# Kernel tuning notes

Hardware: AMD Instinct MI355X
Metric: run time of the kernel (lower is better)

Reference implementation:

```python
import jax, jax.numpy as jnp
import numpy as np

EPS = 1e-8


def setup_inputs() -> dict:
    key = jax.random.key(0)
    k1, k2, k3 = jax.random.split(key, 3)
    B, K, L, D = 4, 64, 128, 768
    context = jax.random.normal(k1, (B, K, 2, L, D), dtype=jnp.float32)
    # MlpModule(input_size=D): Linear(D, D) -> ReLU -> Linear(D, 1)
    w1 = jax.random.normal(k2, (D, D), dtype=jnp.float32) * (1.0 / np.sqrt(D))
    b1 = jnp.zeros((D,), dtype=jnp.float32)
    w2 = jax.random.normal(k3, (D, 1), dtype=jnp.float32) * (1.0 / np.sqrt(D))
    b2 = jnp.zeros((1,), dtype=jnp.float32)
    return {"context": context, "w1": w1, "b1": b1, "w2": w2, "b2": b2}


def reference(context, w1, b1, w2, b2):
    # context: [B, K, 2, L, D]; slice 0 = context tokens, slice 1 = entity tokens
    ctx = context[:, :, 0, :, :]   # [B, K, L, D]
    ent = context[:, :, 1, :, :]   # [B, K, L, D]

    ctx_norm = jnp.linalg.norm(ctx, axis=-1, keepdims=True)  # [B, K, L, 1]
    ent_norm = jnp.linalg.norm(ent, axis=-1, keepdims=True)  # [B, K, L, 1]

    # cosine-similarity score matrix: [B, K, L, L]
    denom = ctx_norm * jnp.swapaxes(ent_norm, -1, -2) + EPS
    scores = jnp.einsum('bkld,bkmd->bklm', ctx, ent) / denom

    # normalized embeddings (torch code does in-place /= before the stack)
    ctx_n = ctx / ctx_norm
    ent_n = ent / ent_norm

    # top-1 match along entity axis, gather matched entity token per context token
    argmax_idx = jnp.argmax(scores, axis=-1)                       # [B, K, L] int
    matched = jnp.take_along_axis(ent_n, argmax_idx[..., None], axis=2)  # [B, K, L, D]

    pair = jnp.stack([ctx_n, matched], axis=-2)  # [B, K, L, 2, D]

    # MLP: Linear(D,D) -> ReLU -> Linear(D,1), then sum over the pair axis
    h = jax.nn.relu(jnp.einsum('bklpd,de->bklpe', pair, w1) + b1)
    out = jnp.einsum('bklpd,do->bklpo', h, w2) + b2   # [B, K, L, 2, 1]
    out = jnp.sum(out, axis=-2)                        # [B, K, L, 1]
    return jnp.squeeze(out, axis=-1)                   # [B, K, L]
```

## Files before the change

kernel.cpp:

```cpp
#include <hip/hip_runtime.h>
#include <hip/hip_bf16.h>
#include <stdint.h>

#define NB 4
#define NK 64
#define NL 128
#define ND 768
#define NBK (NB*NK)
#define NROW (NBK*NL)
#define LD2 (NL*ND)
#define EPSF 1e-8f
#define THETA 2e-3f
#define CAP 16384

typedef __bf16 bf16x8 __attribute__((ext_vector_type(8)));
typedef float  f32x4  __attribute__((ext_vector_type(4)));

__device__ __forceinline__ int row_off(int r) {
  if (r < NROW) return r*ND + (r >> 7)*LD2;
  int r2 = r - NROW;
  return r2*ND + (r2 >> 7)*LD2 + LD2;
}

__global__ __launch_bounds__(256) void k0_w1t(const float* __restrict__ w1,
                                              __bf16* __restrict__ w1t,
                                              unsigned long long* __restrict__ amax2,
                                              unsigned* __restrict__ cntg) {
  __shared__ float tile[64][68];
  int idx = blockIdx.x*256 + threadIdx.x;
  if (idx < NROW) amax2[idx] = 0ull;
  if (idx == 0) *cntg = 0u;
  int kb = (blockIdx.x / 12) * 64, eb = (blockIdx.x % 12) * 64;
  int t = threadIdx.x;
  int r = t >> 2, c0 = (t & 3) * 16;
  #pragma unroll
  for (int j = 0; j < 4; j++) {
    f32x4 v = *(const f32x4*)(w1 + (kb + r)*ND + eb + c0 + j*4);
    *(f32x4*)&tile[r][c0 + j*4] = v;
  }
  __syncthreads();
  int e = t & 63, gi = t >> 6;
  int eg = eb + e;
  #pragma unroll
  for (int g2 = 0; g2 < 2; g2++) {
    int g = gi*2 + g2;
    bf16x8 o;
    #pragma unroll
    for (int j = 0; j < 8; j++) o[j] = (__bf16)tile[g*8 + j][e];
    int G = (kb >> 3) + (g ^ (eg & 7));
    *(bf16x8*)(w1t + eg*ND + G*8) = o;
  }
}

__device__ __forceinline__ void cvt4(f32x4 v, unsigned& hp0, unsigned& hp1,
                                     unsigned& lp0, unsigned& lp1, float& sq) {
  unsigned u0 = __float_as_uint(v[0]), u1 = __float_as_uint(v[1]);
  unsigned u2 = __float_as_uint(v[2]), u3 = __float_as_uint(v[3]);
  hp0 = (u1 & 0xffff0000u) | (u0 >> 16);
  hp1 = (u3 & 0xffff0000u) | (u2 >> 16);
  float l0 = v[0] - __uint_as_float(u0 & 0xffff0000u);
  float l1 = v[1] - __uint_as_float(u1 & 0xffff0000u);
  float l2 = v[2] - __uint_as_float(u2 & 0xffff0000u);
  float l3 = v[3] - __uint_as_float(u3 & 0xffff0000u);
  lp0 = (__float_as_uint(l1) & 0xffff0000u) | (__float_as_uint(l0) >> 16);
  lp1 = (__float_as_uint(l3) & 0xffff0000u) | (__float_as_uint(l2) >> 16);
  sq += v[0]*v[0] + v[1]*v[1] + v[2]*v[2] + v[3]*v[3];
}

__global__ __launch_bounds__(512) void k2a_screen(
    const float* __restrict__ ctxall, float* __restrict__ norm,
    int* __restrict__ amax, unsigned* __restrict__ cntg,
    unsigned* __restrict__ list) {
  __shared__ alignas(16) __bf16 tiles[2][4][128*32];
  __shared__ float einv_s[128];
  int bk = blockIdx.x;
  int t = threadIdx.x;
  int mat = t >> 8, row = (t >> 1) & 127, kh = (t & 1) * 16;
  const float* src = ctxall + bk*2*LD2 + mat*LD2 + row*ND + kh;
  int w = t >> 6, lane = t & 63, quad = lane >> 4, eloc = lane & 15;

  f32x4 pv[4];
  #pragma unroll
  for (int i = 0; i < 4; i++) pv[i] = *(const f32x4*)(src + i*4);
  float sq = 0.f;
  f32x4 acc[8];
  #pragma unroll
  for (int ct = 0; ct < 8; ct++) acc[ct] = (f32x4){0,0,0,0};

  int p = 0;
  for (int kt = 0; kt < 24; kt++) {
    unsigned h0,h1,h2,h3, l0,l1,l2,l3;
    cvt4(pv[0], h0, h1, l0, l1, sq);
    cvt4(pv[1], h2, h3, l2, l3, sq);
    __bf16* hdst = &tiles[p][2*mat  ][row*32 + kh];
    __bf16* ldst = &tiles[p][2*mat+1][row*32 + kh];
    *(uint4*)hdst = make_uint4(h0,h1,h2,h3);
    *(uint4*)ldst = make_uint4(l0,l1,l2,l3);
    cvt4(pv[2], h0, h1, l0, l1, sq);
    cvt4(pv[3], h2, h3, l2, l3, sq);
    *((uint4*)hdst + 1) = make_uint4(h0,h1,h2,h3);
    *((uint4*)ldst + 1) = make_uint4(l0,l1,l2,l3);
    __syncthreads();
    if (kt < 23) {
      const float* s2 = src + (kt+1)*32;
      #pragma unroll
      for (int i = 0; i < 4; i++) pv[i] = *(const f32x4*)(s2 + i*4);
    }
    bf16x8 ah = *(const bf16x8*)&tiles[p][0][(w*16+eloc)*32 + quad*8];
    bf16x8 al = *(const bf16x8*)&tiles[p][1][(w*16+eloc)*32 + quad*8];
    #pragma unroll
    for (int ct = 0; ct < 8; ct++) {
      bf16x8 bh = *(const bf16x8*)&tiles[p][2][(ct*16+eloc)*32 + quad*8];
      bf16x8 bl = *(const bf16x8*)&tiles[p][3][(ct*16+eloc)*32 + quad*8];
      acc[ct] = __builtin_amdgcn_mfma_f32_16x16x32_bf16(al, bh, acc[ct], 0, 0, 0);
      acc[ct] = __builtin_amdgcn_mfma_f32_16x16x32_bf16(ah, bl, acc[ct], 0, 0, 0);
      acc[ct] = __builtin_amdgcn_mfma_f32_16x16x32_bf16(ah, bh, acc[ct], 0, 0, 0);
    }
    p ^= 1;
  }

  float stot = sq + __shfl_xor(sq, 1);
  if ((t & 1) == 0) {
    float n = sqrtf(stot);
    if (mat == 0) norm[bk*NL + row] = n;
    else { norm[NROW + bk*NL + row] = n; einv_s[row] = 1.0f / n; }
  }
  __syncthreads();

  #pragma unroll
  for (int rr = 0; rr < 4; rr++) {
    float sc[8];
    float best = -3.0e38f; int bcol = 0;
    #pragma unroll
    for (int ct = 0; ct < 8; ct++) {
      sc[ct] = acc[ct][rr] * einv_s[ct*16 + eloc];
      int col = ct*16 + eloc;
      if (sc[ct] > best) { best = sc[ct]; bcol = col; }
    }
    #pragma unroll
    for (int m = 1; m < 16; m <<= 1) {
      float ov = __shfl_xor(best, m);
      int   oc = __shfl_xor(bcol, m);
      if (ov > best || (ov == best && oc < bcol)) { best = ov; bcol = oc; }
    }
    int grow = bk*NL + w*16 + quad*4 + rr;
    if (eloc == 0) amax[grow] = bcol;
    int cnt = 0;
    #pragma unroll
    for (int ct = 0; ct < 8; ct++) cnt += (sc[ct] >= best - THETA) ? 1 : 0;
    #pragma unroll
    for (int m = 1; m < 16; m <<= 1) cnt += __shfl_xor(cnt, m);
    if (cnt >= 2) {
      #pragma unroll
      for (int ct = 0; ct < 8; ct++) {
        if (sc[ct] >= best - THETA) {
          unsigned idx = atomicAdd(cntg, 1u);
          if (idx < CAP) list[idx] = ((unsigned)grow << 7) | (unsigned)(ct*16 + eloc);
        }
      }
    }
  }
}

__global__ __launch_bounds__(256) void k2b_rescore(
    const float* __restrict__ ctxall, const float* __restrict__ norm,
    const unsigned* __restrict__ cntg, const unsigned* __restrict__ list,
    unsigned long long* __restrict__ amax2) {
  unsigned n = *cntg; if (n > CAP) n = CAP;
  int lane = threadIdx.x & 63;
  unsigned wv = blockIdx.x*4 + (threadIdx.x >> 6);
  for (unsigned e = wv; e < n; e += 256) {
    unsigned ent = list[e];
    int row = (int)(ent >> 7), col = (int)(ent & 127);
    int bk = row >> 7;
    const float* a = ctxall + row_off(row);
    const float* b = ctxall + bk*2*LD2 + LD2 + col*ND;
    float d = 0.f;
    #pragma unroll
    for (int i = 0; i < 3; i++) {
      f32x4 va = *(const f32x4*)(a + lane*12 + i*4);
      f32x4 vb = *(const f32x4*)(b + lane*12 + i*4);
      d += va[0]*vb[0] + va[1]*vb[1] + va[2]*vb[2] + va[3]*vb[3];
    }
    #pragma unroll
    for (int m = 1; m < 64; m <<= 1) d += __shfl_xor(d, m);
    if (lane == 0) {
      float cn = norm[row], en = norm[NROW + bk*NL + col];
      float s = d / (cn*en + EPSF);
      unsigned su = __float_as_uint(s);
      unsigned ord = (su & 0x80000000u) ? ~su : (su | 0x80000000u);
      unsigned long long key = ((unsigned long long)ord << 32) | (unsigned)(127 - col);
      atomicMax(&amax2[row], key);
    }
  }
}

__global__ __launch_bounds__(256, 2) void k3_mlp(
    const float* __restrict__ ctxall, const float* __restrict__ norm,
    const __bf16* __restrict__ w1t, const float* __restrict__ b1,
    const float* __restrict__ w2, float* __restrict__ val) {
  __shared__ alignas(16) __bf16 btile[2][16*768];
  int tid = threadIdx.x;
  int wave = tid >> 6, lane = tid & 63;
  int quad = lane >> 4, eloc = lane & 15;
  int rbase = blockIdx.x*128 + wave*32;

  #pragma unroll
  for (int i = 0; i < 6; i++) {
    __builtin_amdgcn_global_load_lds(
      (const __attribute__((address_space(1))) unsigned int*)(w1t + (i*256 + tid)*8),
      (__attribute__((address_space(3))) unsigned int*)(&btile[0][0] + (i*256 + tid)*8),
      16, 0, 0);
  }

  bf16x8 afrag[2][24];
  #pragma unroll
  for (int s = 0; s < 2; s++) {
    int r = rbase + s*16 + eloc;
    const float* src = ctxall + row_off(r);
    float rinv = 1.0f / norm[r];
    #pragma unroll
    for (int ks = 0; ks < 24; ks++) {
      const float* sp = src + ks*32 + quad*8;
      f32x4 v0 = *(const f32x4*)sp;
      f32x4 v1 = *(const f32x4*)(sp + 4);
      bf16x8 a;
      a[0] = (__bf16)(v0[0]*rinv); a[1] = (__bf16)(v0[1]*rinv);
      a[2] = (__bf16)(v0[2]*rinv); a[3] = (__bf16)(v0[3]*rinv);
      a[4] = (__bf16)(v1[0]*rinv); a[5] = (__bf16)(v1[1]*rinv);
      a[6] = (__bf16)(v1[2]*rinv); a[7] = (__bf16)(v1[3]*rinv);
      afrag[s][ks] = a;
    }
  }

  float oacc[2][4] = {{0,0,0,0},{0,0,0,0}};
  int p = 0;
  for (int nt = 0; nt < 48; nt++) {
    __syncthreads();
    if (nt < 47) {
      const __bf16* gsrc = w1t + (nt+1)*16*ND;
      #pragma unroll
      for (int i = 0; i < 6; i++) {
        __builtin_amdgcn_global_load_lds(
          (const __attribute__((address_space(1))) unsigned int*)(gsrc + (i*256 + tid)*8),
          (__attribute__((address_space(3))) unsigned int*)(&btile[p^1][0] + (i*256 + tid)*8),
          16, 0, 0);
      }
    }
    f32x4 h0 = {0,0,0,0}, h1 = {0,0,0,0};
    #pragma unroll
    for (int ks = 0; ks < 24; ks++) {
      int g = ks*4 + quad;
      bf16x8 bfrag = *(const bf16x8*)(&btile[p][0] + eloc*ND + ((g ^ (eloc & 7))*8));
      h0 = __builtin_amdgcn_mfma_f32_16x16x32_bf16(afrag[0][ks], bfrag, h0, 0, 0, 0);
      h1 = __builtin_amdgcn_mfma_f32_16x16x32_bf16(afrag[1][ks], bfrag, h1, 0, 0, 0);
    }
    float b1v = b1[nt*16 + eloc];
    float w2v = w2[nt*16 + eloc];
    #pragma unroll
    for (int rr = 0; rr < 4; rr++) {
      oacc[0][rr] += fmaxf(h0[rr] + b1v, 0.f) * w2v;
      oacc[1][rr] += fmaxf(h1[rr] + b1v, 0.f) * w2v;
    }
    p ^= 1;
  }
  #pragma unroll
  for (int m = 1; m < 16; m <<= 1)
    #pragma unroll
    for (int s = 0; s < 2; s++)
      #pragma unroll
      for (int rr = 0; rr < 4; rr++)
        oacc[s][rr] += __shfl_xor(oacc[s][rr], m);
  if (eloc == 0) {
    #pragma unroll
    for (int s = 0; s < 2; s++)
      #pragma unroll
      for (int rr = 0; rr < 4; rr++)
        val[rbase + s*16 + quad*4 + rr] = oacc[s][rr];
  }
}

__global__ void k4_out(const float* __restrict__ val, const int* __restrict__ amax,
                       const unsigned long long* __restrict__ amax2,
                       const float* __restrict__ b2, float* __restrict__ out) {
  int i = blockIdx.x*256 + threadIdx.x;
  int bk = i >> 7;
  unsigned long long k = amax2[i];
  int a = k ? (127 - (int)(k & 127ull)) : amax[i];
  out[i] = val[i] + val[NROW + bk*NL + a] + 2.0f*b2[0];
}

extern "C" void kernel_launch(void* const* d_in, const int* in_sizes, int n_in,
                              void* d_out, int out_size, void* d_ws, size_t ws_size,
                              hipStream_t stream) {
  const float* ctxall = (const float*)d_in[0];
  const float* w1 = (const float*)d_in[1];
  const float* b1 = (const float*)d_in[2];
  const float* w2 = (const float*)d_in[3];
  const float* b2 = (const float*)d_in[4];
  float* out = (float*)d_out;

  char* ws = (char*)d_ws;
  float*    norm = (float*)ws;
  int*      amax = (int*)(ws + 262144);
  float*    val  = (float*)(ws + 393216);
  __bf16*   w1t  = (__bf16*)(ws + 655360);
  unsigned long long* amax2 = (unsigned long long*)(ws + 1835008);
  unsigned* cntg = (unsigned*)(ws + 2097152);
  unsigned* list = (unsigned*)(ws + 2097156);

  hipLaunchKernelGGL(k0_w1t,     dim3(144),        dim3(256), 0, stream, w1, w1t, amax2, cntg);
  hipLaunchKernelGGL(k2a_screen, dim3(NBK),        dim3(512), 0, stream, ctxall, norm, amax, cntg, list);
  hipLaunchKernelGGL(k2b_rescore,dim3(64),         dim3(256), 0, stream, ctxall, norm, cntg, list, amax2);
  hipLaunchKernelGGL(k3_mlp,     dim3(2*NROW/128), dim3(256), 0, stream, ctxall, norm, w1t, b1, w2, val);
  hipLaunchKernelGGL(k4_out,     dim3(NROW/256),   dim3(256), 0, stream, val, amax, amax2, b2, out);
}
```

Baseline: 395.8 us.

## Cache unnormalized bf16 rows in screen kernel and reuse them in MLP kernel

The screen kernel now rounds the fp32 inputs to bf16 with round-to-nearest-even for its hi/lo split and also writes the bf16 hi rows to a workspace buffer. The MLP kernel then reads these bf16 rows instead of re-reading and converting the fp32 context, so it pulls half the bytes. Normalization moves out of the GEMM: the bias is scaled by the row norm before ReLU and the result is divided by the norm afterwards. Each MLP block now handles 256 rows with four accumulator sets to get more reuse of each W1 tile, at the cost of more registers, occupancy 1 and an extra workspace write in the screen kernel.

```diff
diff --git a/kernel.cpp b/kernel.cpp
--- a/kernel.cpp
+++ b/kernel.cpp
@@ -52,31 +52,37 @@
   }
 }
 
+__device__ __forceinline__ unsigned rne_hi(unsigned u) {
+  return (u + 0x7fffu + ((u >> 16) & 1u)) & 0xffff0000u;
+}
 __device__ __forceinline__ void cvt4(f32x4 v, unsigned& hp0, unsigned& hp1,
                                      unsigned& lp0, unsigned& lp1, float& sq) {
-  unsigned u0 = __float_as_uint(v[0]), u1 = __float_as_uint(v[1]);
-  unsigned u2 = __float_as_uint(v[2]), u3 = __float_as_uint(v[3]);
-  hp0 = (u1 & 0xffff0000u) | (u0 >> 16);
-  hp1 = (u3 & 0xffff0000u) | (u2 >> 16);
-  float l0 = v[0] - __uint_as_float(u0 & 0xffff0000u);
-  float l1 = v[1] - __uint_as_float(u1 & 0xffff0000u);
-  float l2 = v[2] - __uint_as_float(u2 & 0xffff0000u);
-  float l3 = v[3] - __uint_as_float(u3 & 0xffff0000u);
-  lp0 = (__float_as_uint(l1) & 0xffff0000u) | (__float_as_uint(l0) >> 16);
-  lp1 = (__float_as_uint(l3) & 0xffff0000u) | (__float_as_uint(l2) >> 16);
+  unsigned r0 = rne_hi(__float_as_uint(v[0]));
+  unsigned r1 = rne_hi(__float_as_uint(v[1]));
+  unsigned r2 = rne_hi(__float_as_uint(v[2]));
+  unsigned r3 = rne_hi(__float_as_uint(v[3]));
+  hp0 = r1 | (r0 >> 16);
+  hp1 = r3 | (r2 >> 16);
+  float l0 = v[0] - __uint_as_float(r0);
+  float l1 = v[1] - __uint_as_float(r1);
+  float l2 = v[2] - __uint_as_float(r2);
+  float l3 = v[3] - __uint_as_float(r3);
+  lp0 = rne_hi(__float_as_uint(l1)) | (rne_hi(__float_as_uint(l0)) >> 16);
+  lp1 = rne_hi(__float_as_uint(l3)) | (rne_hi(__float_as_uint(l2)) >> 16);
   sq += v[0]*v[0] + v[1]*v[1] + v[2]*v[2] + v[3]*v[3];
 }
 
 __global__ __launch_bounds__(512) void k2a_screen(
     const float* __restrict__ ctxall, float* __restrict__ norm,
     int* __restrict__ amax, unsigned* __restrict__ cntg,
-    unsigned* __restrict__ list) {
+    unsigned* __restrict__ list, __bf16* __restrict__ rows8) {
   __shared__ alignas(16) __bf16 tiles[2][4][128*32];
   __shared__ float einv_s[128];
   int bk = blockIdx.x;
   int t = threadIdx.x;
   int mat = t >> 8, row = (t >> 1) & 127, kh = (t & 1) * 16;
   const float* src = ctxall + bk*2*LD2 + mat*LD2 + row*ND + kh;
+  __bf16* rbase8 = rows8 + ((mat ? NROW : 0) + bk*NL + row)*ND + kh;
   int w = t >> 6, lane = t & 63, quad = lane >> 4, eloc = lane & 15;
 
   f32x4 pv[4];
@@ -94,12 +100,15 @@
     cvt4(pv[1], h2, h3, l2, l3, sq);
     __bf16* hdst = &tiles[p][2*mat  ][row*32 + kh];
     __bf16* ldst = &tiles[p][2*mat+1][row*32 + kh];
+    uint4* rdst = (uint4*)(rbase8 + kt*32);
     *(uint4*)hdst = make_uint4(h0,h1,h2,h3);
     *(uint4*)ldst = make_uint4(l0,l1,l2,l3);
+    rdst[0] = make_uint4(h0,h1,h2,h3);
     cvt4(pv[2], h0, h1, l0, l1, sq);
     cvt4(pv[3], h2, h3, l2, l3, sq);
     *((uint4*)hdst + 1) = make_uint4(h0,h1,h2,h3);
     *((uint4*)ldst + 1) = make_uint4(l0,l1,l2,l3);
+    rdst[1] = make_uint4(h0,h1,h2,h3);
     __syncthreads();
     if (kt < 23) {
       const float* s2 = src + (kt+1)*32;
@@ -195,15 +204,15 @@
   }
 }
 
-__global__ __launch_bounds__(256, 2) void k3_mlp(
-    const float* __restrict__ ctxall, const float* __restrict__ norm,
+__global__ __launch_bounds__(256, 1) void k3_mlp(
+    const __bf16* __restrict__ rows8, const float* __restrict__ norm,
     const __bf16* __restrict__ w1t, const float* __restrict__ b1,
     const float* __restrict__ w2, float* __restrict__ val) {
   __shared__ alignas(16) __bf16 btile[2][16*768];
   int tid = threadIdx.x;
   int wave = tid >> 6, lane = tid & 63;
   int quad = lane >> 4, eloc = lane & 15;
-  int rbase = blockIdx.x*128 + wave*32;
+  int rbase = blockIdx.x*256 + wave*64;
 
   #pragma unroll
   for (int i = 0; i < 6; i++) {
@@ -213,27 +222,22 @@
       16, 0, 0);
   }
 
-  bf16x8 afrag[2][24];
-  #pragma unroll
-  for (int s = 0; s < 2; s++) {
-    int r = rbase + s*16 + eloc;
-    const float* src = ctxall + row_off(r);
-    float rinv = 1.0f / norm[r];
-    #pragma unroll
-    for (int ks = 0; ks < 24; ks++) {
-      const float* sp = src + ks*32 + quad*8;
-      f32x4 v0 = *(const f32x4*)sp;
-      f32x4 v1 = *(const f32x4*)(sp + 4);
-      bf16x8 a;
-      a[0] = (__bf16)(v0[0]*rinv); a[1] = (__bf16)(v0[1]*rinv);
-      a[2] = (__bf16)(v0[2]*rinv); a[3] = (__bf16)(v0[3]*rinv);
-      a[4] = (__bf16)(v1[0]*rinv); a[5] = (__bf16)(v1[1]*rinv);
-      a[6] = (__bf16)(v1[2]*rinv); a[7] = (__bf16)(v1[3]*rinv);
-      afrag[s][ks] = a;
-    }
-  }
-
-  float oacc[2][4] = {{0,0,0,0},{0,0,0,0}};
+  bf16x8 afrag[4][24];
+  #pragma unroll
+  for (int s = 0; s < 4; s++) {
+    const __bf16* src = rows8 + (rbase + s*16 + eloc)*ND + quad*8;
+    #pragma unroll
+    for (int ks = 0; ks < 24; ks++)
+      afrag[s][ks] = *(const bf16x8*)(src + ks*32);
+  }
+  float nrm[4][4];
+  #pragma unroll
+  for (int s = 0; s < 4; s++)
+    #pragma unroll
+    for (int rr = 0; rr < 4; rr++)
+      nrm[s][rr] = norm[rbase + s*16 + quad*4 + rr];
+
+  float oacc[4][4] = {{0,0,0,0},{0,0,0,0},{0,0,0,0},{0,0,0,0}};
   int p = 0;
   for (int nt = 0; nt < 48; nt++) {
     __syncthreads();
@@ -247,36 +251,40 @@
           16, 0, 0);
       }
     }
-    f32x4 h0 = {0,0,0,0}, h1 = {0,0,0,0};
+    f32x4 h0 = {0,0,0,0}, h1 = {0,0,0,0}, h2 = {0,0,0,0}, h3 = {0,0,0,0};
     #pragma unroll
     for (int ks = 0; ks < 24; ks++) {
       int g = ks*4 + quad;
       bf16x8 bfrag = *(const bf16x8*)(&btile[p][0] + eloc*ND + ((g ^ (eloc & 7))*8));
       h0 = __builtin_amdgcn_mfma_f32_16x16x32_bf16(afrag[0][ks], bfrag, h0, 0, 0, 0);
       h1 = __builtin_amdgcn_mfma_f32_16x16x32_bf16(afrag[1][ks], bfrag, h1, 0, 0, 0);
+      h2 = __builtin_amdgcn_mfma_f32_16x16x32_bf16(afrag[2][ks], bfrag, h2, 0, 0, 0);
+      h3 = __builtin_amdgcn_mfma_f32_16x16x32_bf16(afrag[3][ks], bfrag, h3, 0, 0, 0);
     }
     float b1v = b1[nt*16 + eloc];
     float w2v = w2[nt*16 + eloc];
     #pragma unroll
     for (int rr = 0; rr < 4; rr++) {
-      oacc[0][rr] += fmaxf(h0[rr] + b1v, 0.f) * w2v;
-      oacc[1][rr] += fmaxf(h1[rr] + b1v, 0.f) * w2v;
+      oacc[0][rr] += fmaxf(h0[rr] + b1v*nrm[0][rr], 0.f) * w2v;
+      oacc[1][rr] += fmaxf(h1[rr] + b1v*nrm[1][rr], 0.f) * w2v;
+      oacc[2][rr] += fmaxf(h2[rr] + b1v*nrm[2][rr], 0.f) * w2v;
+      oacc[3][rr] += fmaxf(h3[rr] + b1v*nrm[3][rr], 0.f) * w2v;
     }
     p ^= 1;
   }
   #pragma unroll
   for (int m = 1; m < 16; m <<= 1)
     #pragma unroll
-    for (int s = 0; s < 2; s++)
+    for (int s = 0; s < 4; s++)
       #pragma unroll
       for (int rr = 0; rr < 4; rr++)
         oacc[s][rr] += __shfl_xor(oacc[s][rr], m);
   if (eloc == 0) {
     #pragma unroll
-    for (int s = 0; s < 2; s++)
+    for (int s = 0; s < 4; s++)
       #pragma unroll
       for (int rr = 0; rr < 4; rr++)
-        val[rbase + s*16 + quad*4 + rr] = oacc[s][rr];
+        val[rbase + s*16 + quad*4 + rr] = oacc[s][rr] / nrm[s][rr];
   }
 }
 
@@ -308,10 +316,11 @@
   unsigned long long* amax2 = (unsigned long long*)(ws + 1835008);
   unsigned* cntg = (unsigned*)(ws + 2097152);
   unsigned* list = (unsigned*)(ws + 2097156);
+  __bf16*   rows8 = (__bf16*)(ws + 4194304);
 
   hipLaunchKernelGGL(k0_w1t,     dim3(144),        dim3(256), 0, stream, w1, w1t, amax2, cntg);
-  hipLaunchKernelGGL(k2a_screen, dim3(NBK),        dim3(512), 0, stream, ctxall, norm, amax, cntg, list);
+  hipLaunchKernelGGL(k2a_screen, dim3(NBK),        dim3(512), 0, stream, ctxall, norm, amax, cntg, list, rows8);
   hipLaunchKernelGGL(k2b_rescore,dim3(64),         dim3(256), 0, stream, ctxall, norm, cntg, list, amax2);
-  hipLaunchKernelGGL(k3_mlp,     dim3(2*NROW/128), dim3(256), 0, stream, ctxall, norm, w1t, b1, w2, val);
+  hipLaunchKernelGGL(k3_mlp,     dim3(256),        dim3(256), 0, stream, rows8, norm, w1t, b1, w2, val);
   hipLaunchKernelGGL(k4_out,     dim3(NROW/256),   dim3(256), 0, stream, val, amax, amax2, b2, out);
 }
```

Result: slower. 442.8 us (+11.9%).
